# Optimization experiments

Measured on AMD Instinct MI355X. Metric: run time of the kernel, lower is better.

The kernel has to match this reference:

```python
import jax, jax.numpy as jnp
import numpy as np

B, SEQ, NF = 16, 512, 32
E, HID, PRED = 128, 512, 96
N_FFT, HOP, TOPM = 64, 32, 32
W = SEQ // HOP + 1          # 17 windows (centered STFT)
F = N_FFT // 2 + 1          # 33 onesided freqs
LAM = 0.01                  # sparsity_threshold (softshrink)
SCALE = 0.02


def _hann(n):
    # periodic hann, matches torch.hann_window default
    return 0.5 - 0.5 * jnp.cos(2.0 * jnp.pi * jnp.arange(n) / n)


def _softshrink(v):
    return jnp.sign(v) * jnp.maximum(jnp.abs(v) - LAM, 0.0)


def setup_inputs():
    key = jax.random.key(0)
    ks = jax.random.split(key, 12)
    d = {}
    d['x'] = jax.random.normal(ks[0], (B, SEQ, NF), jnp.float32)
    d['embeddings'] = jax.random.normal(ks[1], (1, E), jnp.float32)
    for nm, k in zip(['Wr', 'Wi', 'Wrl', 'Wil', 'Wrr', 'Wir'], ks[2:8]):
        d[nm] = SCALE * jax.random.normal(k, (W, E, E), jnp.float32)
    d['br'] = SCALE * jax.random.normal(ks[8], (W, E), jnp.float32)
    d['bi'] = SCALE * jax.random.normal(ks[9], (W, E), jnp.float32)
    d['fc_w1'] = SCALE * jax.random.normal(ks[10], (SEQ * E, HID), jnp.float32)
    d['fc_b1'] = jnp.zeros((HID,), jnp.float32)
    d['fc_w2'] = SCALE * jax.random.normal(ks[11], (HID, PRED), jnp.float32)
    d['fc_b2'] = jnp.zeros((PRED,), jnp.float32)
    return d


def _forward(x, embeddings, Wr, Wi, Wrl, Wil, Wrr, Wir, br, bi,
             fc_w1, fc_b1, fc_w2, fc_b2):
    Bq, T, N = x.shape
    # tokenEmb: (B,T,N) -> (B,N,T,E)
    xe = x.transpose(0, 2, 1)[..., None] * embeddings
    bias = xe
    # ---- STFT (centered, reflect pad, hann, onesided) ----
    xt = xe.transpose(0, 1, 3, 2)                      # (B,N,E,T)
    pad = N_FFT // 2
    xp = jnp.pad(xt, ((0, 0), (0, 0), (0, 0), (pad, pad)), mode='reflect')
    win = _hann(N_FFT).astype(x.dtype)
    idx = jnp.arange(W)[:, None] * HOP + jnp.arange(N_FFT)[None, :]  # (W,nfft)
    frames = xp[..., idx] * win                        # (B,N,E,W,nfft)
    spec = jnp.fft.rfft(frames, axis=-1)               # (B,N,E,W,F)
    spec = spec.transpose(0, 1, 3, 4, 2)               # (B,N,W,F,E)
    # ---- top-M frequency select (dim=3) ----
    sm = jnp.moveaxis(spec, 3, -1)                     # (B,N,W,E,F)
    _, top_idx = jax.lax.top_k(jnp.abs(sm), TOPM)      # (B,N,W,E,M)
    vals = jnp.take_along_axis(sm, top_idx, axis=-1)
    xw = jnp.moveaxis(vals, -1, 3)                     # (B,N,W,M,E)
    # ---- per-window complex MLP with left/right neighbor windows ----
    z0 = jnp.zeros_like(xw[:, :, :1])
    xl = jnp.concatenate([z0, xw[:, :, :-1]], axis=2)  # left neighbor (zero at w=0)
    xr = jnp.concatenate([xw[:, :, 1:], z0], axis=2)   # right neighbor (zero at w=W-1)

    def cmul(z, wr, wi):
        re = jnp.einsum('bnwme,wef->bnwmf', z.real, wr) - jnp.einsum('bnwme,wef->bnwmf', z.imag, wi)
        im = jnp.einsum('bnwme,wef->bnwmf', z.imag, wr) + jnp.einsum('bnwme,wef->bnwmf', z.real, wi)
        return re, im

    re_m, im_m = cmul(xw, Wr, Wi)
    re_l, im_l = cmul(xl, Wrl, Wil)
    re_r, im_r = cmul(xr, Wrr, Wir)
    o_re = jax.nn.relu(re_m + re_l + re_r + br[None, None, :, None, :])
    o_im = jax.nn.relu(im_m + im_l + im_r + bi[None, None, :, None, :])
    y = _softshrink(o_re) + 1j * _softshrink(o_im)     # (B,N,W,M,E) complex
    # ---- scatter-pad back to full frequency grid ----
    ym = jnp.moveaxis(y, 3, -1)                        # (B,N,W,E,M)
    K = Bq * N * W * E
    flat_vals = ym.reshape(K, TOPM)
    flat_idx = top_idx.reshape(K, TOPM)
    full = jnp.zeros((K, F), ym.dtype).at[jnp.arange(K)[:, None], flat_idx].set(flat_vals)
    spec_full = jnp.moveaxis(full.reshape(Bq, N, W, E, F), -1, 3)  # (B,N,W,F,E)
    # ---- ISTFT (windowed OLA / window-squared envelope, centered trim) ----
    sf = spec_full.transpose(0, 1, 4, 2, 3)            # (B,N,E,W,F)
    fr = jnp.fft.irfft(sf, n=N_FFT, axis=-1) * win     # (B,N,E,W,nfft)
    L = (W - 1) * HOP + N_FFT
    ola = jnp.zeros((Bq, N, E, L), fr.dtype).at[..., idx].add(fr)
    env = jnp.zeros((L,), win.dtype).at[idx].add(win * win)
    ola = ola / jnp.where(env > 1e-11, env, 1.0)
    xt2 = ola[..., pad:L - pad]                        # (B,N,E,T)
    xo = xt2.transpose(0, 1, 3, 2) + bias              # (B,N,T,E) + residual
    # ---- fc head ----
    h = xo.reshape(Bq, N, T * E)
    h = jax.nn.leaky_relu(h @ fc_w1 + fc_b1, 0.01)
    out = h @ fc_w2 + fc_b2                            # (B,N,PRED)
    return out.transpose(0, 2, 1)                      # (B,PRED,N)


def reference(x, embeddings, Wr, Wi, Wrl, Wil, Wrr, Wir, br, bi,
              fc_w1, fc_b1, fc_w2, fc_b2):
    return _forward(x, embeddings, Wr, Wi, Wrl, Wil, Wrr, Wir, br, bi,
                    fc_w1, fc_b1, fc_w2, fc_b2)
```

## Files before the change

kernel.cpp:

```cpp
#include <hip/hip_runtime.h>
#include <hip/hip_bf16.h>

#define LAM 0.01f

typedef __attribute__((ext_vector_type(8))) short v8s;
typedef __attribute__((ext_vector_type(4))) float v4f;

static __device__ __forceinline__ unsigned short f2bf(float f) {
    union { float f; unsigned int u; } v; v.f = f;
    unsigned int u = v.u;
    u += 0x7fffu + ((u >> 16) & 1u);
    return (unsigned short)(u >> 16);
}
static __device__ __forceinline__ float bf2f(unsigned short h) {
    union { unsigned int u; float f; } c; c.u = ((unsigned int)h) << 16;
    return c.f;
}
static __device__ __forceinline__ unsigned int pkbf(float a, float b) {
    union { __hip_bfloat162 h; unsigned int u; } c;
    c.h = __float22bfloat162_rn(float2{a, b});
    return c.u;
}

static __device__ __forceinline__ void async16(const void* g, void* l) {
    __builtin_amdgcn_global_load_lds(
        (const __attribute__((address_space(1))) unsigned int*)g,
        (__attribute__((address_space(3))) unsigned int*)l, 16, 0, 0);
}

#define OFF_COEF 0ull
#define OFF_V    69632ull
#define OFF_BINS 2297856ull
#define OFF_AIMG 3411968ull
#define OFF_W1P  70520832ull
#define OFF_HP   137629696ull

__global__ __launch_bounds__(256) void pre_kernel(
    const float* __restrict__ w1, unsigned short* __restrict__ w1p,
    const float* __restrict__ emb,
    const float* __restrict__ Wr, const float* __restrict__ Wi,
    const float* __restrict__ Wrl, const float* __restrict__ Wil,
    const float* __restrict__ Wrr, const float* __restrict__ Wir,
    const float* __restrict__ br, const float* __restrict__ bi,
    float* __restrict__ coef,
    const float* __restrict__ x, float2* __restrict__ V, int* __restrict__ bins)
{
    __shared__ __align__(16) float smem[4096];

    const int tid = threadIdx.x;
    const int bid = blockIdx.x;

    if (bid < 68) {
        const int pair = bid * 2 + (tid >> 7);
        const int w = pair >> 3, j = pair & 7, e = tid & 127;
        float out;
        if (j < 6) {
            const float* Wj;
            switch (j) {
                case 0: Wj = Wr; break; case 1: Wj = Wi; break;
                case 2: Wj = Wrl; break; case 3: Wj = Wil; break;
                case 4: Wj = Wrr; break; default: Wj = Wir; break;
            }
            const float* p = Wj + (size_t)w * 16384 + e;
            float acc = 0.f;
            #pragma unroll 8
            for (int ep = 0; ep < 128; ++ep) acc = fmaf(emb[ep], p[ep * 128], acc);
            out = acc;
        } else if (j == 6) {
            out = br[w * 128 + e] - LAM;
        } else {
            out = bi[w * 128 + e] - LAM;
        }
        coef[((size_t)(w * 128 + e)) * 8 + j] = out;
        return;
    }

    if (bid < 1092) {
        float* sigL  = smem;
        float* winT  = smem + 336;
        float2* tw   = (float2*)(smem + 400);
        float2* Sbuf = (float2*)(smem + 528);
        float* absb  = smem + 1122;

        const int blk = bid - 68;
        const int bn = blk >> 1, wh = blk & 1;
        const int b = bn >> 5, n = bn & 31;
        const int w0 = wh ? 9 : 0;
        const int nW = wh ? 8 : 9;
        const int sbase = wh ? 288 : 0;
        const int slen = wh ? 288 : 320;
        const float C64 = 0.09817477042468103f;

        if (tid < 64) {
            float ang = (float)tid * C64;
            winT[tid] = 0.5f - 0.5f * cosf(ang);
            tw[tid] = make_float2(cosf(ang), sinf(ang));
        }
        for (int l = tid; l < slen; l += 256) {
            int g = sbase + l;
            int t = (g < 32) ? (32 - g) : ((g < 544) ? (g - 32) : (1054 - g));
            sigL[l] = x[(size_t)b * 16384 + t * 32 + n];
        }
        __syncthreads();

        const int ntask = nW * 33;
        for (int task = tid; task < ntask; task += 256) {
            int wl = task / 33, f = task - wl * 33;
            float sr = 0.f, si = 0.f;
            int base = (w0 + wl) * 32 - sbase;
            for (int t = 0; t < 64; ++t) {
                float sw = sigL[base + t] * winT[t];
                float2 cs = tw[(f * t) & 63];
                sr = fmaf(sw, cs.x, sr);
                si = fmaf(sw, -cs.y, si);
            }
            Sbuf[task] = make_float2(sr, si);
            absb[task] = sqrtf(fmaf(sr, sr, si * si));
        }
        __syncthreads();

        for (int task = tid; task < ntask; task += 256) {
            int wl = task / 33, f = task - wl * 33;
            float a = absb[task];
            int base = wl * 33, rank = 0;
            for (int j = 0; j < 33; ++j) {
                float aj = absb[base + j];
                rank += (aj > a) || (aj == a && j < f);
            }
            if (rank < 32) {
                size_t o = ((size_t)bn * 17 + (w0 + wl)) * 32 + rank;
                V[o] = Sbuf[task];
                bins[o] = f;
            }
        }
        return;
    }

    const int cb = bid - 1092;
    const int kb = cb & 2047, nt = cb >> 11;
    const int wv = tid >> 6, lane = tid & 63;

    #pragma unroll
    for (int j = 0; j < 4; ++j) {
        int r = wv * 8 + j * 2 + (lane >> 5);
        int g = (lane & 31) ^ (wv * 2);
        const float* src = w1 + ((size_t)(kb * 32 + r)) * 512 + nt * 128 + g * 4;
        async16(src, (char*)smem + wv * 4096 + j * 1024);
    }
    asm volatile("s_waitcnt vmcnt(0)" ::: "memory");
    __syncthreads();

    unsigned short* dst = w1p + ((size_t)nt * 2048 + kb) * 4096;
    #pragma unroll
    for (int p = 0; p < 2; ++p) {
        int pos = tid + 256 * p;
        int np = pos >> 2, cs = pos & 3;
        int clog = cs ^ ((np >> 2) & 3);
        int gsw = (((np >> 2) ^ (clog << 1)) << 2) + (np & 3);
        unsigned int pk[4];
        #pragma unroll
        for (int j2 = 0; j2 < 4; ++j2) {
            int r0 = clog * 8 + j2 * 2;
            float a = smem[r0 * 128 + gsw];
            float b = smem[(r0 + 1) * 128 + gsw];
            pk[j2] = pkbf(a, b);
        }
        *(uint4*)&dst[pos * 8] = make_uint4(pk[0], pk[1], pk[2], pk[3]);
    }
}

#define MID_ROLL(J0, J1, J2, J3)                                                \
    {                                                                           \
        _Pragma("unroll") for (int e2 = 0; e2 < 2; ++e2)                        \
        _Pragma("unroll") for (int i = 0; i < 4; ++i) {                         \
            roll[e2][J0][i] = fmaf(acc[0][e2][i], win16[0][i], roll[e2][J0][i]);\
            roll[e2][J1][i] = fmaf(acc[1][e2][i], win16[1][i], roll[e2][J1][i]);\
            roll[e2][J2][i] = fmaf(acc[2][e2][i], win16[2][i], roll[e2][J2][i]);\
            roll[e2][J3][i] = fmaf(acc[3][e2][i], win16[3][i], roll[e2][J3][i]);\
        }                                                                       \
    }

#define MID_FLUSH(JJA, JJB)                                                     \
    {                                                                           \
        _Pragma("unroll") for (int i = 0; i < 4; ++i) {                         \
            int tp = 32 * (w - 1) + q * 4 + i;                                  \
            float xb = xs[tp];                                                  \
            _Pragma("unroll") for (int e2 = 0; e2 < 2; ++e2) {                  \
                float val = fmaf(roll[e2][JJA][i], renv[0][i], xb * emb2[e2]);  \
                Aimg[cbase[e2] + (size_t)tp * 16384] = f2bf(val);               \
                roll[e2][JJA][i] = 0.f;                                         \
            }                                                                   \
            int tp2 = tp + 16;                                                  \
            float xb2 = xs[tp2];                                                \
            _Pragma("unroll") for (int e2 = 0; e2 < 2; ++e2) {                  \
                float val = fmaf(roll[e2][JJB][i], renv[1][i], xb2 * emb2[e2]); \
                Aimg[cbase[e2] + (size_t)tp2 * 16384] = f2bf(val);              \
                roll[e2][JJB][i] = 0.f;                                         \
            }                                                                   \
        }                                                                       \
    }

__global__ __launch_bounds__(256) void mid_kernel(
    const float* __restrict__ x, const float* __restrict__ emb,
    const float* __restrict__ coef, const float2* __restrict__ V,
    const int* __restrict__ bins, unsigned short* __restrict__ Aimg)
{
    __shared__ unsigned short M1t[2][64 * 72];
    __shared__ unsigned short Yt[2][128 * 72];
    __shared__ float cosT[64];
    __shared__ float sinT[64];
    __shared__ float2 Vs2[19 * 32];
    __shared__ int Bns[17 * 32];
    __shared__ float xs[512];

    const int blk = blockIdx.x;
    const int b = blk >> 5, n = blk & 31;
    const int tid = threadIdx.x;
    const int wave = tid >> 6, lane = tid & 63, l15 = lane & 15, q = lane >> 4;
    const float C64 = 0.09817477042468103f;

    if (tid < 64) {
        float ang = (float)tid * C64;
        cosT[tid] = __cosf(ang);
        sinT[tid] = __sinf(ang);
    }
    {
        const float2* Vg = V + (size_t)blk * 544;
        const int* Bg = bins + (size_t)blk * 544;
        for (int i = tid; i < 544; i += 256) { Vs2[32 + i] = Vg[i]; Bns[i] = Bg[i]; }
        if (tid < 64) {
            int r = (tid < 32) ? tid : (18 * 32 + tid - 32);
            Vs2[r] = make_float2(0.f, 0.f);
        }
        for (int i = tid; i < 512; i += 256) xs[i] = x[(size_t)b * 16384 + i * 32 + n];
    }

    float win16[4][4];
    #pragma unroll
    for (int tt = 0; tt < 4; ++tt)
        #pragma unroll
        for (int i = 0; i < 4; ++i) {
            int t = tt * 16 + q * 4 + i;
            win16[tt][i] = 0.5f - 0.5f * __cosf((float)t * C64);
        }
    float renv[2][4];
    #pragma unroll
    for (int hf = 0; hf < 2; ++hf)
        #pragma unroll
        for (int i = 0; i < 4; ++i) {
            int k = hf * 16 + q * 4 + i;
            float w0 = 0.5f - 0.5f * __cosf((float)k * C64);
            float w1v = 0.5f - 0.5f * __cosf((float)(k + 32) * C64);
            renv[hf][i] = 1.0f / (w0 * w0 + w1v * w1v);
        }
    int ebase[2];
    float emb2[2];
    size_t cbase[2];
    const int mt = blk >> 7, mp = blk & 127, s = (mp >> 2) & 3;
    #pragma unroll
    for (int e2 = 0; e2 < 2; ++e2) {
        ebase[e2] = (wave * 2 + e2) * 16 + l15;
        emb2[e2] = emb[ebase[e2]];
        int e = ebase[e2];
        int echunk = e >> 5, clog = (e >> 3) & 3, cs = clog ^ s, el = e & 7;
        cbase[e2] = ((size_t)mt * 2048 + echunk) * 4096 + mp * 32 + cs * 8 + el;
    }

    float roll[2][4][4];
    #pragma unroll
    for (int e2 = 0; e2 < 2; ++e2)
        #pragma unroll
        for (int jj = 0; jj < 4; ++jj)
            #pragma unroll
            for (int i = 0; i < 4; ++i) roll[e2][jj][i] = 0.f;

    const int e1 = tid & 127;
    const int mg = (tid >> 7) << 4;
    const int tM = tid & 63;
    const int kg = wave << 4;

    __syncthreads();

    for (int w = 0; w < 17; ++w) {
        const int buf = w & 1;
        {
            const float4* cf = (const float4*)(coef + ((size_t)(w * 128 + e1)) * 8);
            float4 cA = cf[0];
            float4 cB = cf[1];
            unsigned int rep[8], imp[8];
            #pragma unroll
            for (int j2 = 0; j2 < 8; ++j2) {
                float rev[2], imv[2];
                #pragma unroll
                for (int sdx = 0; sdx < 2; ++sdx) {
                    int m = mg + j2 * 2 + sdx;
                    float2 vm = Vs2[(w + 1) * 32 + m];
                    float2 vl = Vs2[w * 32 + m];
                    float2 vp = Vs2[(w + 2) * 32 + m];
                    float re = cB.z;
                    re = fmaf(vm.x, cA.x, re); re = fmaf(-vm.y, cA.y, re);
                    re = fmaf(vl.x, cA.z, re); re = fmaf(-vl.y, cA.w, re);
                    re = fmaf(vp.x, cB.x, re); re = fmaf(-vp.y, cB.y, re);
                    float im = cB.w;
                    im = fmaf(vm.y, cA.x, im); im = fmaf(vm.x, cA.y, im);
                    im = fmaf(vl.y, cA.z, im); im = fmaf(vl.x, cA.w, im);
                    im = fmaf(vp.y, cB.x, im); im = fmaf(vp.x, cB.y, im);
                    rev[sdx] = fmaxf(re, 0.f);
                    imv[sdx] = fmaxf(im, 0.f);
                }
                rep[j2] = pkbf(rev[0], rev[1]);
                imp[j2] = pkbf(imv[0], imv[1]);
            }
            uint4* dr = (uint4*)&Yt[buf][e1 * 72 + mg];
            dr[0] = make_uint4(rep[0], rep[1], rep[2], rep[3]);
            dr[1] = make_uint4(rep[4], rep[5], rep[6], rep[7]);
            uint4* di = (uint4*)&Yt[buf][e1 * 72 + 32 + mg];
            di[0] = make_uint4(imp[0], imp[1], imp[2], imp[3]);
            di[1] = make_uint4(imp[4], imp[5], imp[6], imp[7]);
        }
        {
            unsigned int mpk[8];
            #pragma unroll
            for (int j2 = 0; j2 < 8; ++j2) {
                float vv[2];
                #pragma unroll
                for (int sdx = 0; sdx < 2; ++sdx) {
                    int k = kg + j2 * 2 + sdx;
                    int m = k & 31;
                    int r = Bns[w * 32 + m];
                    float sc = (r == 0 || r == 32) ? 0.015625f : 0.03125f;
                    int idx = (r * tM) & 63;
                    vv[sdx] = (k < 32) ? (cosT[idx] * sc) : (-sinT[idx] * sc);
                }
                mpk[j2] = pkbf(vv[0], vv[1]);
            }
            uint4* dm = (uint4*)&M1t[buf][tM * 72 + kg];
            dm[0] = make_uint4(mpk[0], mpk[1], mpk[2], mpk[3]);
            dm[1] = make_uint4(mpk[4], mpk[5], mpk[6], mpk[7]);
        }
        __syncthreads();

        v4f acc[4][2];
        #pragma unroll
        for (int tt = 0; tt < 4; ++tt)
            #pragma unroll
            for (int e2 = 0; e2 < 2; ++e2) acc[tt][e2] = (v4f){0.f, 0.f, 0.f, 0.f};
        #pragma unroll
        for (int ks = 0; ks < 2; ++ks) {
            v8s bfr[2];
            #pragma unroll
            for (int e2 = 0; e2 < 2; ++e2)
                bfr[e2] = *(const v8s*)&Yt[buf][ebase[e2] * 72 + ks * 32 + q * 8];
            #pragma unroll
            for (int tt = 0; tt < 4; ++tt) {
                v8s af = *(const v8s*)&M1t[buf][(tt * 16 + l15) * 72 + ks * 32 + q * 8];
                #pragma unroll
                for (int e2 = 0; e2 < 2; ++e2)
                    acc[tt][e2] = __builtin_amdgcn_mfma_f32_16x16x32_bf16(
                        af, bfr[e2], acc[tt][e2], 0, 0, 0);
            }
        }

        if ((w & 1) == 0) {
            MID_ROLL(0, 1, 2, 3);
            if (w > 0) {
                MID_FLUSH(0, 1);
            } else {
                #pragma unroll
                for (int e2 = 0; e2 < 2; ++e2)
                    #pragma unroll
                    for (int i = 0; i < 4; ++i) {
                        roll[e2][0][i] = 0.f; roll[e2][1][i] = 0.f;
                    }
            }
        } else {
            MID_ROLL(2, 3, 0, 1);
            MID_FLUSH(2, 3);
        }
    }
}

__global__ __launch_bounds__(512) void gemm_kernel(
    const unsigned short* __restrict__ Aimg, const unsigned short* __restrict__ w1p,
    unsigned short* __restrict__ hp, int iters, int KS)
{
    __shared__ unsigned short As[3][8192];
    __shared__ unsigned short Bs[3][8192];

    const int gid = blockIdx.x;
    const int xcd = gid & 7;
    const int idx = gid >> 3;
    const int ks = xcd * (KS >> 3) + (idx >> 2);
    const int quad = idx & 3;
    const int mt2 = quad & 1;
    const int nt2 = quad >> 1;

    const int tid = threadIdx.x;
    const int wave = tid >> 6, lane = tid & 63;
    const int l15 = lane & 15, q = lane >> 4;
    const int kb0 = ks * iters;

    const int isB = wave >> 2;
    const int sub = wave & 3;
    const unsigned short* gsrc = (isB
        ? w1p + ((size_t)(nt2 * 2 + (sub >> 1)) * 2048 + kb0) * 4096
        : Aimg + ((size_t)(mt2 * 2 + (sub >> 1)) * 2048 + kb0) * 4096)
        + (sub & 1) * 2048 + lane * 8;
    const int ldsoff = (sub >> 1) * 4096 + (sub & 1) * 2048;

    v4f acc[4][8];
    #pragma unroll
    for (int mf = 0; mf < 4; ++mf)
        #pragma unroll
        for (int nf = 0; nf < 8; ++nf) acc[mf][nf] = (v4f){0.f, 0.f, 0.f, 0.f};

    {
        unsigned short* dst0 = (isB ? Bs[0] : As[0]) + ldsoff;
        #pragma unroll
        for (int j = 0; j < 4; ++j) async16(gsrc + j * 512, dst0 + j * 512);
        if (iters > 1) {
            const unsigned short* s1 = gsrc + 4096;
            unsigned short* dst1 = (isB ? Bs[1] : As[1]) + ldsoff;
            #pragma unroll
            for (int j = 0; j < 4; ++j) async16(s1 + j * 512, dst1 + j * 512);
        }
    }

    const int wm = wave >> 1, wn = wave & 1;
    const int ca = (q ^ ((l15 >> 2) & 3)) * 8;
    const int rA = (wm >> 1) * 4096 + ((wm & 1) * 64 + l15) * 32 + ca;
    const int rB = wn * 4096 + l15 * 32 + ca;

    for (int it = 0; it < iters; ++it) {
        if (it + 1 < iters) {
            asm volatile("s_waitcnt vmcnt(4)" ::: "memory");
        } else {
            asm volatile("s_waitcnt vmcnt(0)" ::: "memory");
        }
        __builtin_amdgcn_s_barrier();
        __builtin_amdgcn_sched_barrier(0);
        if (it + 2 < iters) {
            const int nb = (it + 2) % 3;
            const unsigned short* src = gsrc + (size_t)(it + 2) * 4096;
            unsigned short* dst = (isB ? Bs[nb] : As[nb]) + ldsoff;
            #pragma unroll
            for (int j = 0; j < 4; ++j) async16(src + j * 512, dst + j * 512);
        }
        const int cur = it % 3;
        v8s af[4], bf[8];
        #pragma unroll
        for (int f = 0; f < 4; ++f) af[f] = *(const v8s*)&As[cur][rA + f * 512];
        #pragma unroll
        for (int nf = 0; nf < 8; ++nf) bf[nf] = *(const v8s*)&Bs[cur][rB + nf * 512];
        #pragma unroll
        for (int mf = 0; mf < 4; ++mf)
            #pragma unroll
            for (int nf = 0; nf < 8; ++nf)
                acc[mf][nf] = __builtin_amdgcn_mfma_f32_16x16x32_bf16(
                    af[mf], bf[nf], acc[mf][nf], 0, 0, 0);
    }

    #pragma unroll
    for (int mf = 0; mf < 4; ++mf)
        #pragma unroll
        for (int nf = 0; nf < 8; ++nf) {
            int row = mt2 * 256 + wm * 64 + mf * 16 + q * 4;
            int col = nt2 * 256 + wn * 128 + nf * 16 + l15;
            unsigned short* dst = hp + ((size_t)row * KS + ks) * 512 + col;
            #pragma unroll
            for (int i = 0; i < 4; ++i)
                dst[(size_t)i * KS * 512] = f2bf(acc[mf][nf][i]);
        }
}

__global__ __launch_bounds__(256) void fc2_kernel(
    const unsigned short* __restrict__ hp, const float* __restrict__ b1,
    const float* __restrict__ w2, const float* __restrict__ b2,
    float* __restrict__ out, int KS)
{
    __shared__ float hbuf[512];
    __shared__ float part[2][96];
    const int row = blockIdx.x;
    const int tid = threadIdx.x;

    const unsigned int* base = (const unsigned int*)(hp + (size_t)row * KS * 512) + tid;
    float a0 = 0.f, a1 = 0.f;
    #pragma unroll 8
    for (int k = 0; k < KS; ++k) {
        unsigned int v = base[k * 256];
        a0 += bf2f((unsigned short)(v & 0xffff));
        a1 += bf2f((unsigned short)(v >> 16));
    }
    float s0 = a0 + b1[tid * 2];
    float s1 = a1 + b1[tid * 2 + 1];
    hbuf[tid * 2]     = (s0 > 0.f) ? s0 : 0.01f * s0;
    hbuf[tid * 2 + 1] = (s1 > 0.f) ? s1 : 0.01f * s1;
    __syncthreads();

    if (tid < 192) {
        const int c = (tid >= 96) ? 1 : 0;
        const int o = tid - 96 * c;
        float a = 0.f;
        #pragma unroll 8
        for (int h = c * 256; h < c * 256 + 256; ++h)
            a = fmaf(hbuf[h], w2[h * 96 + o], a);
        part[c][o] = a;
    }
    __syncthreads();

    if (tid < 96) {
        float a = part[0][tid] + part[1][tid] + b2[tid];
        int b = row >> 5, n = row & 31;
        out[(size_t)b * 3072 + tid * 32 + n] = a;
    }
}

extern "C" void kernel_launch(void* const* d_in, const int* in_sizes, int n_in,
                              void* d_out, int out_size, void* d_ws, size_t ws_size,
                              hipStream_t stream) {
    const float* x   = (const float*)d_in[0];
    const float* emb = (const float*)d_in[1];
    const float* Wr  = (const float*)d_in[2];
    const float* Wi  = (const float*)d_in[3];
    const float* Wrl = (const float*)d_in[4];
    const float* Wil = (const float*)d_in[5];
    const float* Wrr = (const float*)d_in[6];
    const float* Wir = (const float*)d_in[7];
    const float* br  = (const float*)d_in[8];
    const float* bi  = (const float*)d_in[9];
    const float* w1  = (const float*)d_in[10];
    const float* b1  = (const float*)d_in[11];
    const float* w2  = (const float*)d_in[12];
    const float* b2  = (const float*)d_in[13];

    char* ws = (char*)d_ws;
    float* coef          = (float*)(ws + OFF_COEF);
    float2* V            = (float2*)(ws + OFF_V);
    int* bins            = (int*)(ws + OFF_BINS);
    unsigned short* Aimg = (unsigned short*)(ws + OFF_AIMG);
    unsigned short* w1p  = (unsigned short*)(ws + OFF_W1P);
    unsigned short* hpp  = (unsigned short*)(ws + OFF_HP);

    int KS = 64;
    size_t hp_bytes = (size_t)KS * 512 * 512 * 2;
    if (OFF_HP + hp_bytes > ws_size) {
        KS = 32; hp_bytes = (size_t)KS * 512 * 512 * 2;
    }
    int iters = 2048 / KS;

    pre_kernel<<<dim3(9284), dim3(256), 0, stream>>>(
        w1, w1p, emb, Wr, Wi, Wrl, Wil, Wrr, Wir, br, bi, coef, x, V, bins);
    mid_kernel<<<dim3(512), dim3(256), 0, stream>>>(x, emb, coef, V, bins, Aimg);
    gemm_kernel<<<dim3(4 * KS), dim3(512), 0, stream>>>(Aimg, w1p, hpp, iters, KS);
    fc2_kernel<<<dim3(512), dim3(256), 0, stream>>>(hpp, b1, w2, b2, (float*)d_out, KS);
}
```

Baseline: 365.0 us.

## Fuse fc_w1 bf16 conversion into GEMM B-tile loads, dropping pre-pass copy

Removes the separate pre-pass that converted and swizzled the fp32 fc_w1 weight into a bf16 workspace image. The GEMM kernel now loads fp32 weights directly into registers, packs them to bf16 and writes them into LDS after the MFMA block, overlapping the loads with compute. This avoids writing and re-reading about 64 MB of intermediate weights, at the cost of extra register pressure and global loads that are not async LDS copies inside the GEMM loop.

Result: slower. 383.5 us (+5.1%).

```diff
diff --git a/kernel.cpp b/kernel.cpp
--- a/kernel.cpp
+++ b/kernel.cpp
@@ -32,11 +32,9 @@
 #define OFF_V    69632ull
 #define OFF_BINS 2297856ull
 #define OFF_AIMG 3411968ull
-#define OFF_W1P  70520832ull
 #define OFF_HP   137629696ull
 
 __global__ __launch_bounds__(256) void pre_kernel(
-    const float* __restrict__ w1, unsigned short* __restrict__ w1p,
     const float* __restrict__ emb,
     const float* __restrict__ Wr, const float* __restrict__ Wi,
     const float* __restrict__ Wrl, const float* __restrict__ Wil,
@@ -45,7 +43,7 @@
     float* __restrict__ coef,
     const float* __restrict__ x, float2* __restrict__ V, int* __restrict__ bins)
 {
-    __shared__ __align__(16) float smem[4096];
+    __shared__ __align__(16) float smem[1424];
 
     const int tid = threadIdx.x;
     const int bid = blockIdx.x;
@@ -75,97 +73,62 @@
         return;
     }
 
-    if (bid < 1092) {
-        float* sigL  = smem;
-        float* winT  = smem + 336;
-        float2* tw   = (float2*)(smem + 400);
-        float2* Sbuf = (float2*)(smem + 528);
-        float* absb  = smem + 1122;
-
-        const int blk = bid - 68;
-        const int bn = blk >> 1, wh = blk & 1;
-        const int b = bn >> 5, n = bn & 31;
-        const int w0 = wh ? 9 : 0;
-        const int nW = wh ? 8 : 9;
-        const int sbase = wh ? 288 : 0;
-        const int slen = wh ? 288 : 320;
-        const float C64 = 0.09817477042468103f;
-
-        if (tid < 64) {
-            float ang = (float)tid * C64;
-            winT[tid] = 0.5f - 0.5f * cosf(ang);
-            tw[tid] = make_float2(cosf(ang), sinf(ang));
-        }
-        for (int l = tid; l < slen; l += 256) {
-            int g = sbase + l;
-            int t = (g < 32) ? (32 - g) : ((g < 544) ? (g - 32) : (1054 - g));
-            sigL[l] = x[(size_t)b * 16384 + t * 32 + n];
-        }
-        __syncthreads();
-
-        const int ntask = nW * 33;
-        for (int task = tid; task < ntask; task += 256) {
-            int wl = task / 33, f = task - wl * 33;
-            float sr = 0.f, si = 0.f;
-            int base = (w0 + wl) * 32 - sbase;
-            for (int t = 0; t < 64; ++t) {
-                float sw = sigL[base + t] * winT[t];
-                float2 cs = tw[(f * t) & 63];
-                sr = fmaf(sw, cs.x, sr);
-                si = fmaf(sw, -cs.y, si);
-            }
-            Sbuf[task] = make_float2(sr, si);
-            absb[task] = sqrtf(fmaf(sr, sr, si * si));
-        }
-        __syncthreads();
-
-        for (int task = tid; task < ntask; task += 256) {
-            int wl = task / 33, f = task - wl * 33;
-            float a = absb[task];
-            int base = wl * 33, rank = 0;
-            for (int j = 0; j < 33; ++j) {
-                float aj = absb[base + j];
-                rank += (aj > a) || (aj == a && j < f);
-            }
-            if (rank < 32) {
-                size_t o = ((size_t)bn * 17 + (w0 + wl)) * 32 + rank;
-                V[o] = Sbuf[task];
-                bins[o] = f;
-            }
-        }
-        return;
-    }
-
-    const int cb = bid - 1092;
-    const int kb = cb & 2047, nt = cb >> 11;
-    const int wv = tid >> 6, lane = tid & 63;
-
-    #pragma unroll
-    for (int j = 0; j < 4; ++j) {
-        int r = wv * 8 + j * 2 + (lane >> 5);
-        int g = (lane & 31) ^ (wv * 2);
-        const float* src = w1 + ((size_t)(kb * 32 + r)) * 512 + nt * 128 + g * 4;
-        async16(src, (char*)smem + wv * 4096 + j * 1024);
-    }
-    asm volatile("s_waitcnt vmcnt(0)" ::: "memory");
+    float* sigL  = smem;
+    float* winT  = smem + 336;
+    float2* tw   = (float2*)(smem + 400);
+    float2* Sbuf = (float2*)(smem + 528);
+    float* absb  = smem + 1122;
+
+    const int blk = bid - 68;
+    const int bn = blk >> 1, wh = blk & 1;
+    const int b = bn >> 5, n = bn & 31;
+    const int w0 = wh ? 9 : 0;
+    const int nW = wh ? 8 : 9;
+    const int sbase = wh ? 288 : 0;
+    const int slen = wh ? 288 : 320;
+    const float C64 = 0.09817477042468103f;
+
+    if (tid < 64) {
+        float ang = (float)tid * C64;
+        winT[tid] = 0.5f - 0.5f * cosf(ang);
+        tw[tid] = make_float2(cosf(ang), sinf(ang));
+    }
+    for (int l = tid; l < slen; l += 256) {
+        int g = sbase + l;
+        int t = (g < 32) ? (32 - g) : ((g < 544) ? (g - 32) : (1054 - g));
+        sigL[l] = x[(size_t)b * 16384 + t * 32 + n];
+    }
     __syncthreads();
 
-    unsigned short* dst = w1p + ((size_t)nt * 2048 + kb) * 4096;
-    #pragma unroll
-    for (int p = 0; p < 2; ++p) {
-        int pos = tid + 256 * p;
-        int np = pos >> 2, cs = pos & 3;
-        int clog = cs ^ ((np >> 2) & 3);
-        int gsw = (((np >> 2) ^ (clog << 1)) << 2) + (np & 3);
-        unsigned int pk[4];
-        #pragma unroll
-        for (int j2 = 0; j2 < 4; ++j2) {
-            int r0 = clog * 8 + j2 * 2;
-            float a = smem[r0 * 128 + gsw];
-            float b = smem[(r0 + 1) * 128 + gsw];
-            pk[j2] = pkbf(a, b);
-        }
-        *(uint4*)&dst[pos * 8] = make_uint4(pk[0], pk[1], pk[2], pk[3]);
+    const int ntask = nW * 33;
+    for (int task = tid; task < ntask; task += 256) {
+        int wl = task / 33, f = task - wl * 33;
+        float sr = 0.f, si = 0.f;
+        int base = (w0 + wl) * 32 - sbase;
+        for (int t = 0; t < 64; ++t) {
+            float sw = sigL[base + t] * winT[t];
+            float2 cs = tw[(f * t) & 63];
+            sr = fmaf(sw, cs.x, sr);
+            si = fmaf(sw, -cs.y, si);
+        }
+        Sbuf[task] = make_float2(sr, si);
+        absb[task] = sqrtf(fmaf(sr, sr, si * si));
+    }
+    __syncthreads();
+
+    for (int task = tid; task < ntask; task += 256) {
+        int wl = task / 33, f = task - wl * 33;
+        float a = absb[task];
+        int base = wl * 33, rank = 0;
+        for (int j = 0; j < 33; ++j) {
+            float aj = absb[base + j];
+            rank += (aj > a) || (aj == a && j < f);
+        }
+        if (rank < 32) {
+            size_t o = ((size_t)bn * 17 + (w0 + wl)) * 32 + rank;
+            V[o] = Sbuf[task];
+            bins[o] = f;
+        }
     }
 }
 
@@ -381,7 +344,7 @@
 }
 
 __global__ __launch_bounds__(512) void gemm_kernel(
-    const unsigned short* __restrict__ Aimg, const unsigned short* __restrict__ w1p,
+    const unsigned short* __restrict__ Aimg, const float* __restrict__ w1,
     unsigned short* __restrict__ hp, int iters, int KS)
 {
     __shared__ unsigned short As[3][8192];
@@ -402,11 +365,16 @@
 
     const int isB = wave >> 2;
     const int sub = wave & 3;
-    const unsigned short* gsrc = (isB
-        ? w1p + ((size_t)(nt2 * 2 + (sub >> 1)) * 2048 + kb0) * 4096
-        : Aimg + ((size_t)(mt2 * 2 + (sub >> 1)) * 2048 + kb0) * 4096)
+    const unsigned short* gsrcA = Aimg
+        + ((size_t)(mt2 * 2 + (sub >> 1)) * 2048 + kb0) * 4096
         + (sub & 1) * 2048 + lane * 8;
     const int ldsoff = (sub >> 1) * 4096 + (sub & 1) * 2048;
+
+    const int ntq = nt2 * 2 + (sub >> 1);
+    const int pos0 = (sub & 1) * 256 + lane;
+    const int np0 = pos0 >> 2, cs0 = pos0 & 3;
+    const int clogB = cs0 ^ ((np0 >> 2) & 3);
+    const float* bbase = w1 + (size_t)(clogB * 8) * 512 + ntq * 128 + np0;
 
     v4f acc[4][8];
     #pragma unroll
@@ -414,15 +382,38 @@
         #pragma unroll
         for (int nf = 0; nf < 8; ++nf) acc[mf][nf] = (v4f){0.f, 0.f, 0.f, 0.f};
 
-    {
-        unsigned short* dst0 = (isB ? Bs[0] : As[0]) + ldsoff;
-        #pragma unroll
-        for (int j = 0; j < 4; ++j) async16(gsrc + j * 512, dst0 + j * 512);
+    float bv[4][8];
+
+    if (isB) {
+        #pragma unroll
+        for (int s2 = 0; s2 < 2; ++s2) {
+            if (s2 < iters) {
+                const float* src = bbase + (size_t)(kb0 + s2) * 16384;
+                #pragma unroll
+                for (int j = 0; j < 4; ++j)
+                    #pragma unroll
+                    for (int r = 0; r < 8; ++r)
+                        bv[j][r] = src[(size_t)r * 512 + j * 16];
+                #pragma unroll
+                for (int j = 0; j < 4; ++j) {
+                    unsigned int p0 = pkbf(bv[j][0], bv[j][1]);
+                    unsigned int p1 = pkbf(bv[j][2], bv[j][3]);
+                    unsigned int p2 = pkbf(bv[j][4], bv[j][5]);
+                    unsigned int p3 = pkbf(bv[j][6], bv[j][7]);
+                    *(uint4*)&Bs[s2][ldsoff + j * 512 + lane * 8] =
+                        make_uint4(p0, p1, p2, p3);
+                }
+            }
+        }
+    } else {
+        #pragma unroll
+        for (int j = 0; j < 4; ++j)
+            async16(gsrcA + j * 512, As[0] + ldsoff + j * 512);
         if (iters > 1) {
-            const unsigned short* s1 = gsrc + 4096;
-            unsigned short* dst1 = (isB ? Bs[1] : As[1]) + ldsoff;
-            #pragma unroll
-            for (int j = 0; j < 4; ++j) async16(s1 + j * 512, dst1 + j * 512);
+            const unsigned short* s1 = gsrcA + 4096;
+            #pragma unroll
+            for (int j = 0; j < 4; ++j)
+                async16(s1 + j * 512, As[1] + ldsoff + j * 512);
         }
     }
 
@@ -432,6 +423,7 @@
     const int rB = wn * 4096 + l15 * 32 + ca;
 
     for (int it = 0; it < iters; ++it) {
+        asm volatile("s_waitcnt lgkmcnt(0)" ::: "memory");
         if (it + 1 < iters) {
             asm volatile("s_waitcnt vmcnt(4)" ::: "memory");
         } else {
@@ -439,12 +431,22 @@
         }
         __builtin_amdgcn_s_barrier();
         __builtin_amdgcn_sched_barrier(0);
-        if (it + 2 < iters) {
-            const int nb = (it + 2) % 3;
-            const unsigned short* src = gsrc + (size_t)(it + 2) * 4096;
-            unsigned short* dst = (isB ? Bs[nb] : As[nb]) + ldsoff;
-            #pragma unroll
-            for (int j = 0; j < 4; ++j) async16(src + j * 512, dst + j * 512);
+        const int nb = (it + 2) % 3;
+        const bool st = (it + 2 < iters);
+        if (st) {
+            if (isB) {
+                const float* src = bbase + (size_t)(kb0 + it + 2) * 16384;
+                #pragma unroll
+                for (int j = 0; j < 4; ++j)
+                    #pragma unroll
+                    for (int r = 0; r < 8; ++r)
+                        bv[j][r] = src[(size_t)r * 512 + j * 16];
+            } else {
+                const unsigned short* src = gsrcA + (size_t)(it + 2) * 4096;
+                #pragma unroll
+                for (int j = 0; j < 4; ++j)
+                    async16(src + j * 512, As[nb] + ldsoff + j * 512);
+            }
         }
         const int cur = it % 3;
         v8s af[4], bf[8];
@@ -458,6 +460,17 @@
             for (int nf = 0; nf < 8; ++nf)
                 acc[mf][nf] = __builtin_amdgcn_mfma_f32_16x16x32_bf16(
                     af[mf], bf[nf], acc[mf][nf], 0, 0, 0);
+        if (st && isB) {
+            #pragma unroll
+            for (int j = 0; j < 4; ++j) {
+                unsigned int p0 = pkbf(bv[j][0], bv[j][1]);
+                unsigned int p1 = pkbf(bv[j][2], bv[j][3]);
+                unsigned int p2 = pkbf(bv[j][4], bv[j][5]);
+                unsigned int p3 = pkbf(bv[j][6], bv[j][7]);
+                *(uint4*)&Bs[nb][ldsoff + j * 512 + lane * 8] =
+                    make_uint4(p0, p1, p2, p3);
+            }
+        }
     }
 
     #pragma unroll
@@ -538,7 +551,6 @@
     float2* V            = (float2*)(ws + OFF_V);
     int* bins            = (int*)(ws + OFF_BINS);
     unsigned short* Aimg = (unsigned short*)(ws + OFF_AIMG);
-    unsigned short* w1p  = (unsigned short*)(ws + OFF_W1P);
     unsigned short* hpp  = (unsigned short*)(ws + OFF_HP);
 
     int KS = 64;
@@ -548,9 +560,9 @@
     }
     int iters = 2048 / KS;
 
-    pre_kernel<<<dim3(9284), dim3(256), 0, stream>>>(
-        w1, w1p, emb, Wr, Wi, Wrl, Wil, Wrr, Wir, br, bi, coef, x, V, bins);
+    pre_kernel<<<dim3(1092), dim3(256), 0, stream>>>(
+        emb, Wr, Wi, Wrl, Wil, Wrr, Wir, br, bi, coef, x, V, bins);
     mid_kernel<<<dim3(512), dim3(256), 0, stream>>>(x, emb, coef, V, bins, Aimg);
-    gemm_kernel<<<dim3(4 * KS), dim3(512), 0, stream>>>(Aimg, w1p, hpp, iters, KS);
+    gemm_kernel<<<dim3(4 * KS), dim3(512), 0, stream>>>(Aimg, w1, hpp, iters, KS);
     fc2_kernel<<<dim3(512), dim3(256), 0, stream>>>(hpp, b1, w2, b2, (float*)d_out, KS);
 }
```
